# Optimization experiments

Hardware: AMD Instinct MI355X
Metric: run time of the kernel (lower is better)

Reference implementation:

```python
import jax, jax.numpy as jnp
import numpy as np

N = 768      # n_proto (number of class prototypes)
D = 128      # trans_feat_num
H = D // 16  # edge-MLP hidden = 8
A = 312      # semantic attribute dim
INIT_TEMP = 0.1
VTEMP = 10.0
STEMP = 10.0
EPS = 1e-8


def _layer_norm(x, g, b, eps=1e-5):
    m = x.mean(-1, keepdims=True)
    v = ((x - m) ** 2).mean(-1, keepdims=True)
    return (x - m) / jnp.sqrt(v + eps) * g + b


def _instance_norm_rows(x, eps=1e-5):
    # torch InstanceNorm1d on 2D input: unbatched (C, L) -> normalize each row, no affine
    m = x.mean(-1, keepdims=True)
    v = ((x - m) ** 2).mean(-1, keepdims=True)
    return (x - m) / jnp.sqrt(v + eps)


def _init_edge(x, temp):
    # pairwise cosine similarity + row softmax
    nrm = jnp.linalg.norm(x, axis=1)
    sim = (x @ x.T) / jnp.maximum(nrm[:, None] * nrm[None, :], EPS)
    return jax.nn.softmax(sim / temp, axis=-1)


def _edge_update(proto, last_edge, W1, b1, W2, b2, temp):
    n, d = proto.shape
    # O(n^2) pairwise squared differences  -> [n*n, d]
    feat = ((proto[:, None, :] - proto[None, :, :]) ** 2).reshape(n * n, d)
    h = jax.nn.relu(_instance_norm_rows(feat @ W1.T + b1))  # [n*n, H]
    e = jnp.tanh(h @ W2.T + b2).reshape(n, n)
    return jax.nn.softmax(e * (last_edge + EPS) / temp, axis=-1)


def _node_update(proto, last_edge, edge, W, b, g, beta):
    extra = last_edge @ proto          # cross-modal message (dist_injection)
    p = edge @ proto                   # same-modal aggregation
    return jax.nn.relu(_layer_norm((p + extra) @ W.T + b, g, beta)) + p


def setup_inputs() -> dict:
    key = jax.random.key(0)
    ks = jax.random.split(key, 9)
    rn = lambda k, shape, s=1.0: jax.random.normal(k, shape, dtype=jnp.float32) * s
    return {
        "visual_proto": rn(ks[0], (N, D)),
        "semantic_proto": rn(ks[1], (N, D)),
        "attribute": rn(ks[2], (N, A)),
        "Wvn": rn(ks[3], (D, D), 0.08), "bvn": jnp.zeros((D,), jnp.float32),
        "gvn": jnp.ones((D,), jnp.float32), "betavn": jnp.zeros((D,), jnp.float32),
        "Wve1": rn(ks[4], (H, D), 0.1), "bve1": jnp.zeros((H,), jnp.float32),
        "Wve2": rn(ks[5], (1, H), 0.3), "bve2": jnp.zeros((1,), jnp.float32),
        "Wsn": rn(ks[6], (D, D), 0.08), "bsn": jnp.zeros((D,), jnp.float32),
        "gsn": jnp.ones((D,), jnp.float32), "betasn": jnp.zeros((D,), jnp.float32),
        "Wse1": rn(ks[7], (H, D), 0.1), "bse1": jnp.zeros((H,), jnp.float32),
        "Wse2": rn(ks[8], (1, H), 0.3), "bse2": jnp.zeros((1,), jnp.float32),
    }


def reference(visual_proto, semantic_proto, attribute,
              Wvn, bvn, gvn, betavn, Wve1, bve1, Wve2, bve2,
              Wsn, bsn, gsn, betasn, Wse1, bse1, Wse2, bse2):
    ve = _init_edge(visual_proto, INIT_TEMP)
    se = _init_edge(attribute, INIT_TEMP)
    vp = _node_update(visual_proto, se, ve, Wvn, bvn, gvn, betavn)
    ve2 = _edge_update(vp, ve, Wve1, bve1, Wve2, bve2, VTEMP)
    sp = _node_update(semantic_proto, ve2, se, Wsn, bsn, gsn, betasn)
    se2 = _edge_update(sp, se, Wse1, bse1, Wse2, bse2, STEMP)
    return vp, sp, ve2, se2
```

## Files before the change

### kernel.cpp

```cpp
#include <hip/hip_runtime.h>
#include <math.h>

#define NN 768
#define DD 128
#define AA 312
#define HH 8
#define CEPS 1e-8f
#define SMEM_F 5920

typedef __attribute__((ext_vector_type(8))) short s8b;
typedef __attribute__((ext_vector_type(4))) float f4v;

__device__ __forceinline__ float wave_sum(float v) {
    #pragma unroll
    for (int o = 32; o; o >>= 1) v += __shfl_down(v, o, 64);
    return v;
}
__device__ __forceinline__ float wave_max(float v) {
    #pragma unroll
    for (int o = 32; o; o >>= 1) v = fmaxf(v, __shfl_down(v, o, 64));
    return v;
}
__device__ __forceinline__ unsigned short f2bf(float f) {
    unsigned u = __float_as_uint(f);
    u += 0x7FFFu + ((u >> 16) & 1u);
    return (unsigned short)(u >> 16);
}

struct KParams {
    const float *visual, *semantic, *attribute;
    const float *Wvn, *bvn, *gvn, *betavn, *Wve1, *bve1, *Wve2, *bve2;
    const float *Wsn, *bsn, *gsn, *betasn, *Wse1, *bse1, *Wse2, *bse2;
    float *vp, *sp, *ve2, *se2;
    float *simv, *sima, *WvnT, *WsnT, *cvec1, *cvec2;
    float *nrmv, *nrma;
    short *vpb, *spb;
};

__global__ __launch_bounds__(256) void gram_mfma_kernel(KParams p) {
    __shared__ __align__(16) unsigned short AH[64 * 40];
    __shared__ __align__(16) unsigned short AL[64 * 40];
    __shared__ __align__(16) unsigned short BH[64 * 40];
    __shared__ __align__(16) unsigned short BL[64 * 40];
    const int task = blockIdx.x;
    const int tid = threadIdx.x;
    if (task < 288) {
        const bool isv = (task < 144);
        const int tt = isv ? task : task - 144;
        const int bi = tt / 12, bj = tt % 12;
        const float* M = isv ? p.visual : p.attribute;
        float* G = isv ? p.simv : p.sima;
        float* nrm = isv ? p.nrmv : p.nrma;
        const int K = isv ? DD : AA;
        const int i0 = bi * 64, j0 = bj * 64;
        const int w = tid >> 6, lane = tid & 63;
        const int m = lane & 15, q = lane >> 4;
        f4v acc[4] = {{0.f, 0.f, 0.f, 0.f}, {0.f, 0.f, 0.f, 0.f},
                      {0.f, 0.f, 0.f, 0.f}, {0.f, 0.f, 0.f, 0.f}};
        const int nchunk = (K + 31) >> 5;
        const int srow = tid >> 2, sq = (tid & 3) * 8;
        for (int c = 0; c < nchunk; ++c) {
            const int kc = c * 32;
            __syncthreads();
            #pragma unroll
            for (int h = 0; h < 2; ++h) {
                const int col = sq + h * 4;
                float4 a = {0.f, 0.f, 0.f, 0.f}, b = {0.f, 0.f, 0.f, 0.f};
                if (kc + col + 4 <= K) {
                    a = *(const float4*)(M + (size_t)(i0 + srow) * K + kc + col);
                    b = *(const float4*)(M + (size_t)(j0 + srow) * K + kc + col);
                }
                const float av[4] = {a.x, a.y, a.z, a.w};
                const float bv[4] = {b.x, b.y, b.z, b.w};
                #pragma unroll
                for (int e = 0; e < 4; ++e) {
                    const unsigned short ah = f2bf(av[e]);
                    const float ahf = __uint_as_float((unsigned)ah << 16);
                    const unsigned short al = f2bf(av[e] - ahf);
                    const unsigned short bh = f2bf(bv[e]);
                    const float bhf = __uint_as_float((unsigned)bh << 16);
                    const unsigned short bl = f2bf(bv[e] - bhf);
                    AH[srow * 40 + col + e] = ah;
                    AL[srow * 40 + col + e] = al;
                    BH[srow * 40 + col + e] = bh;
                    BL[srow * 40 + col + e] = bl;
                }
            }
            __syncthreads();
            const s8b ah8 = *(const s8b*)&AH[(w * 16 + m) * 40 + q * 8];
            const s8b al8 = *(const s8b*)&AL[(w * 16 + m) * 40 + q * 8];
            #pragma unroll
            for (int jt = 0; jt < 4; ++jt) {
                const s8b bh8 = *(const s8b*)&BH[(jt * 16 + m) * 40 + q * 8];
                const s8b bl8 = *(const s8b*)&BL[(jt * 16 + m) * 40 + q * 8];
                acc[jt] = __builtin_amdgcn_mfma_f32_16x16x32_bf16(ah8, bh8, acc[jt], 0, 0, 0);
                acc[jt] = __builtin_amdgcn_mfma_f32_16x16x32_bf16(ah8, bl8, acc[jt], 0, 0, 0);
                acc[jt] = __builtin_amdgcn_mfma_f32_16x16x32_bf16(al8, bh8, acc[jt], 0, 0, 0);
            }
        }
        #pragma unroll
        for (int jt = 0; jt < 4; ++jt) {
            #pragma unroll
            for (int r = 0; r < 4; ++r) {
                G[(size_t)(i0 + w * 16 + q * 4 + r) * NN + j0 + jt * 16 + m] = acc[jt][r];
                if (bi == bj && jt == w && m == q * 4 + r)
                    nrm[i0 + w * 16 + m] = sqrtf(fmaxf(acc[jt][r], 0.f));
            }
        }
    } else {
        float* smem = (float*)AH;
        const int u = task - 288;
        const float* S = (u >= 16) ? p.Wsn : p.Wvn;
        float* Dt = (u >= 16) ? p.WsnT : p.WvnT;
        const int tile = u & 15;
        const int c0 = (tile & 3) * 32, r0 = (tile >> 2) * 32;
        const int tx = tid & 31, ty = tid >> 5;
        #pragma unroll
        for (int rr = ty; rr < 32; rr += 8)
            smem[rr * 33 + tx] = S[(size_t)(r0 + rr) * DD + c0 + tx];
        __syncthreads();
        #pragma unroll
        for (int rr = ty; rr < 32; rr += 8)
            Dt[(size_t)(c0 + rr) * DD + r0 + tx] = smem[tx * 33 + rr];
    }
}

__device__ void block_softmax768(float* buf, int tid, float* red) {
    const int w = tid >> 6, lane = tid & 63;
    float v0 = buf[tid];
    float v1 = (tid < NN - 512) ? buf[tid + 512] : -3.4e38f;
    float m = wave_max(fmaxf(v0, v1));
    if (lane == 0) red[w] = m;
    __syncthreads();
    m = red[0];
    #pragma unroll
    for (int i = 1; i < 8; ++i) m = fmaxf(m, red[i]);
    float e0 = __expf(v0 - m);
    float e1 = (tid < NN - 512) ? __expf(v1 - m) : 0.f;
    float sw = wave_sum(e0 + e1);
    if (lane == 0) red[8 + w] = sw;
    __syncthreads();
    float s = 0.f;
    #pragma unroll
    for (int i = 0; i < 8; ++i) s += red[8 + i];
    const float inv = 1.f / s;
    buf[tid] = e0 * inv;
    if (tid < NN - 512) buf[tid + 512] = e1 * inv;
    __syncthreads();
}

__device__ void norm_rows(float (*buf)[NN], const float* __restrict__ nrm, int i0, int tid) {
    const float n0 = nrm[i0], n1 = nrm[i0 + 1];
    for (int k = tid; k < NN; k += 512) {
        const float nj = nrm[k];
        buf[0][k] = buf[0][k] * 10.f / fmaxf(n0 * nj, CEPS);
        buf[1][k] = buf[1][k] * 10.f / fmaxf(n1 * nj, CEPS);
    }
}

template <bool SMEP, bool SMEX>
__global__ __launch_bounds__(512) void node_kernel(
    const float* __restrict__ P, const float* __restrict__ EpSrc, const float* __restrict__ ExSrc,
    const float* __restrict__ nrmP, const float* __restrict__ nrmX,
    const float* __restrict__ WT, const float* __restrict__ b, const float* __restrict__ g,
    const float* __restrict__ beta, float* __restrict__ out, const float* __restrict__ W1e,
    short* __restrict__ outb, float* __restrict__ cvec) {
    __shared__ __align__(16) float ep[2][NN], ex[2][NN];
    __shared__ __align__(16) float pp[4][2][DD], xx[4][2][DD];
    __shared__ __align__(16) float qs[2][DD], tps[2][2][DD];
    __shared__ float red[16];
    const int i0 = blockIdx.x * 2;
    const int tid = threadIdx.x;
    const int s = (tid >> 7) & 3, d = tid & 127;
    if (tid < 384) {
        ((float4*)ep)[tid] = ((const float4*)(EpSrc + (size_t)i0 * NN))[tid];
        ((float4*)ex)[tid] = ((const float4*)(ExSrc + (size_t)i0 * NN))[tid];
    }
    __syncthreads();
    if (SMEP) {
        norm_rows(ep, nrmP, i0, tid);
        block_softmax768(ep[0], tid, red);
        block_softmax768(ep[1], tid, red);
    }
    if (SMEX) {
        norm_rows(ex, nrmX, i0, tid);
        block_softmax768(ex[0], tid, red);
        block_softmax768(ex[1], tid, red);
    }
    float p0 = 0.f, x0 = 0.f, p1 = 0.f, x1 = 0.f;
    const int kb = s * 192;
    #pragma unroll 4
    for (int kk = 0; kk < 192; ++kk) {
        const int k = kb + kk;
        const float pv = P[(size_t)k * DD + d];
        p0 = fmaf(ep[0][k], pv, p0);
        x0 = fmaf(ex[0][k], pv, x0);
        p1 = fmaf(ep[1][k], pv, p1);
        x1 = fmaf(ex[1][k], pv, x1);
    }
    pp[s][0][d] = p0; xx[s][0][d] = x0;
    pp[s][1][d] = p1; xx[s][1][d] = x1;
    __syncthreads();
    const int rr = (tid >> 7) & 1;
    float preg = 0.f;
    if (tid < 256) {
        float p = pp[0][rr][d] + pp[1][rr][d] + pp[2][rr][d] + pp[3][rr][d];
        float x = xx[0][rr][d] + xx[1][rr][d] + xx[2][rr][d] + xx[3][rr][d];
        qs[rr][d] = p + x;
        preg = p;
    }
    __syncthreads();
    {
        const int sc = tid >> 8, rr2 = (tid >> 7) & 1;
        float t = (sc == 0) ? b[d] : 0.f;
        const int c0 = sc * 64;
        #pragma unroll 4
        for (int c = c0; c < c0 + 64; ++c) t = fmaf(qs[rr2][c], WT[(size_t)c * DD + d], t);
        tps[sc][rr2][d] = t;
    }
    __syncthreads();
    float tval = 0.f;
    if (tid < 256) tval = tps[0][rr][d] + tps[1][rr][d];
    float sm = wave_sum(tid < 256 ? tval : 0.f);
    if ((tid & 63) == 0) red[tid >> 6] = sm;
    __syncthreads();
    if (tid < 256) tval -= (red[2 * rr] + red[2 * rr + 1]) * (1.f / DD);
    float s2 = wave_sum(tid < 256 ? tval * tval : 0.f);
    if ((tid & 63) == 0) red[8 + (tid >> 6)] = s2;
    __syncthreads();
    if (tid < 256) {
        const float var = (red[8 + 2 * rr] + red[8 + 2 * rr + 1]) * (1.f / DD);
        const float ln = tval * rsqrtf(var + 1e-5f) * g[d] + beta[d];
        const float val = fmaxf(ln, 0.f) + preg;
        out[(size_t)(i0 + rr) * DD + d] = val;
        outb[(size_t)(i0 + rr) * DD + d] = (short)f2bf(val);
        qs[rr][d] = val;
    }
    __syncthreads();
    if (tid < 256) {
        const int row = tid >> 7, r = (tid >> 4) & 7, l16 = tid & 15;
        float ssum = 0.f;
        #pragma unroll
        for (int t = 0; t < 8; ++t) {
            const int k = l16 + 16 * t;
            const float pv = qs[row][k];
            ssum = fmaf(W1e[r * DD + k], pv * pv, ssum);
        }
        #pragma unroll
        for (int o = 8; o; o >>= 1) ssum += __shfl_down(ssum, o, 16);
        if (l16 == 0) cvec[(size_t)(i0 + row) * HH + r] = ssum;
    }
}

__global__ __launch_bounds__(512) void edge_kernel(
    const float* __restrict__ PR, const short* __restrict__ PRb, const float* __restrict__ cvec,
    const float* __restrict__ ELraw, const float* __restrict__ nrmE,
    const float* __restrict__ W1, const float* __restrict__ b1, const float* __restrict__ W2,
    const float* __restrict__ b2, float invtemp, float* __restrict__ out) {
    __shared__ __align__(16) float pi[2][DD];
    __shared__ __align__(16) float w1s[HH * DD];
    __shared__ __align__(16) short a_sw[4 * 64 * 8];
    __shared__ __align__(16) float Ls[2][NN];
    __shared__ __align__(16) float Els[2][NN];
    __shared__ float red[16];
    const int i0 = blockIdx.x * 2;
    const int tid = threadIdx.x;
    const int lane = tid & 63, wave = tid >> 6;
    if (tid < 256) {
        pi[tid >> 7][tid & 127] = PR[(size_t)(i0 + (tid >> 7)) * DD + (tid & 127)];
        ((float4*)w1s)[tid] = ((const float4*)W1)[tid];
    }
    if (tid < 384)
        ((float4*)Els)[tid] = ((const float4*)(ELraw + (size_t)i0 * NN))[tid];
    __syncthreads();
    norm_rows(Els, nrmE, i0, tid);
    block_softmax768(Els[0], tid, red);
    block_softmax768(Els[1], tid, red);
    if (tid < 256) {
        const int t = tid >> 6, m = lane & 15, q2 = lane >> 4;
        const int il = m >> 3, r = m & 7;
        const int kb = t * 32 + q2 * 8;
        s8b av;
        #pragma unroll
        for (int e = 0; e < 8; ++e)
            av[e] = (short)f2bf(pi[il][kb + e] * w1s[r * DD + kb + e]);
        *(s8b*)&a_sw[(t * 64 + lane) * 8] = av;
    }
    __syncthreads();
    s8b af[4];
    #pragma unroll
    for (int t = 0; t < 4; ++t) af[t] = *(const s8b*)&a_sw[(t * 64 + lane) * 8];
    const int q = lane >> 4, n = lane & 15;
    const int rbase = (q & 1) * 4;
    const int il = q >> 1;
    const float4 ci4 = *(const float4*)&cvec[(size_t)(i0 + il) * HH + rbase];
    const float4 b14 = *(const float4*)&b1[rbase];
    const float4 w24 = *(const float4*)&W2[rbase];
    const float b2s = b2[0];
    #pragma unroll
    for (int s = 0; s < 6; ++s) {
        const int j = wave * 96 + s * 16 + n;
        f4v acc = {0.f, 0.f, 0.f, 0.f};
        #pragma unroll
        for (int t = 0; t < 4; ++t) {
            const s8b bf = *(const s8b*)(PRb + (size_t)j * DD + t * 32 + q * 8);
            acc = __builtin_amdgcn_mfma_f32_16x16x32_bf16(af[t], bf, acc, 0, 0, 0);
        }
        const float4 cj = *(const float4*)&cvec[(size_t)j * HH + rbase];
        float z[4];
        z[0] = ci4.x + cj.x - 2.f * acc[0] + b14.x;
        z[1] = ci4.y + cj.y - 2.f * acc[1] + b14.y;
        z[2] = ci4.z + cj.z - 2.f * acc[2] + b14.z;
        z[3] = ci4.w + cj.w - 2.f * acc[3] + b14.w;
        float s1 = z[0] + z[1] + z[2] + z[3];
        float s2 = z[0] * z[0] + z[1] * z[1] + z[2] * z[2] + z[3] * z[3];
        s1 += __shfl_xor(s1, 16, 64);
        s2 += __shfl_xor(s2, 16, 64);
        const float mean = s1 * (1.f / HH);
        const float var = fmaxf(s2 * (1.f / HH) - mean * mean, 0.f);
        const float istd = rsqrtf(var + 1e-5f);
        float a2 = 0.f;
        a2 = fmaf(fmaxf((z[0] - mean) * istd, 0.f), w24.x, a2);
        a2 = fmaf(fmaxf((z[1] - mean) * istd, 0.f), w24.y, a2);
        a2 = fmaf(fmaxf((z[2] - mean) * istd, 0.f), w24.z, a2);
        a2 = fmaf(fmaxf((z[3] - mean) * istd, 0.f), w24.w, a2);
        a2 += __shfl_xor(a2, 16, 64);
        const float tv = tanhf(a2 + b2s);
        const float lv = Els[il][j];
        if ((q & 1) == 0) Ls[il][j] = tv * (lv + CEPS) * invtemp;
    }
    __syncthreads();
    block_softmax768(Ls[0], tid, red);
    block_softmax768(Ls[1], tid, red);
    float* d0 = out + (size_t)i0 * NN;
    float* d1 = out + (size_t)(i0 + 1) * NN;
    d0[tid] = Ls[0][tid];
    d1[tid] = Ls[1][tid];
    if (tid < NN - 512) {
        d0[tid + 512] = Ls[0][tid + 512];
        d1[tid + 512] = Ls[1][tid + 512];
    }
}

extern "C" void kernel_launch(void* const* d_in, const int* in_sizes, int n_in, void* d_out,
                              int out_size, void* d_ws, size_t ws_size, hipStream_t stream) {
    KParams kp;
    kp.visual    = (const float*)d_in[0];
    kp.semantic  = (const float*)d_in[1];
    kp.attribute = (const float*)d_in[2];
    kp.Wvn  = (const float*)d_in[3];
    kp.bvn  = (const float*)d_in[4];
    kp.gvn  = (const float*)d_in[5];
    kp.betavn = (const float*)d_in[6];
    kp.Wve1 = (const float*)d_in[7];
    kp.bve1 = (const float*)d_in[8];
    kp.Wve2 = (const float*)d_in[9];
    kp.bve2 = (const float*)d_in[10];
    kp.Wsn  = (const float*)d_in[11];
    kp.bsn  = (const float*)d_in[12];
    kp.gsn  = (const float*)d_in[13];
    kp.betasn = (const float*)d_in[14];
    kp.Wse1 = (const float*)d_in[15];
    kp.bse1 = (const float*)d_in[16];
    kp.Wse2 = (const float*)d_in[17];
    kp.bse2 = (const float*)d_in[18];

    float* out = (float*)d_out;
    kp.vp  = out;
    kp.sp  = out + 98304;
    kp.ve2 = out + 196608;
    kp.se2 = out + 786432;

    float* ws = (float*)d_ws;
    kp.simv  = ws;
    kp.sima  = ws + 589824;
    kp.WvnT  = ws + 2949120;
    kp.WsnT  = ws + 2965504;
    kp.cvec1 = ws + 2981888;
    kp.cvec2 = ws + 2988032;
    kp.vpb   = (short*)(ws + 2994176);
    kp.spb   = (short*)(ws + 3043328);
    kp.nrmv  = ws + 3092480;
    kp.nrma  = ws + 3093248;

    gram_mfma_kernel<<<320, 256, 0, stream>>>(kp);
    node_kernel<true, true><<<NN / 2, 512, 0, stream>>>(
        kp.visual, kp.simv, kp.sima, kp.nrmv, kp.nrma, kp.WvnT, kp.bvn, kp.gvn, kp.betavn,
        kp.vp, kp.Wve1, kp.vpb, kp.cvec1);
    edge_kernel<<<NN / 2, 512, 0, stream>>>(kp.vp, kp.vpb, kp.cvec1, kp.simv, kp.nrmv, kp.Wve1,
                                            kp.bve1, kp.Wve2, kp.bve2, 0.1f, kp.ve2);
    node_kernel<true, false><<<NN / 2, 512, 0, stream>>>(
        kp.semantic, kp.sima, kp.ve2, kp.nrma, nullptr, kp.WsnT, kp.bsn, kp.gsn, kp.betasn,
        kp.sp, kp.Wse1, kp.spb, kp.cvec2);
    edge_kernel<<<NN / 2, 512, 0, stream>>>(kp.sp, kp.spb, kp.cvec2, kp.sima, kp.nrma, kp.Wse1,
                                            kp.bse1, kp.Wse2, kp.bse2, 0.1f, kp.se2);
}
```

Measured before the change: 190.4 us.

## Fuse edge update with next node update and cache initial edge softmaxes

Merges the first edge-update kernel with the semantic node-update kernel, so the freshly computed ve2 rows feed the node aggregation directly from shared memory instead of a global round trip and a separate launch. The node1 kernel now stores the softmaxed initial edge rows (ve, se) to workspace, so later kernels reload them rather than recomputing the norm and softmax. This cuts one kernel launch and redundant softmax work. In exchange it uses extra global traffic for the cached edges and more LDS per block in the fused kernel, which may reduce occupancy.

```diff
diff --git a/kernel.cpp b/kernel.cpp
--- a/kernel.cpp
+++ b/kernel.cpp
@@ -6,7 +6,6 @@
 #define AA 312
 #define HH 8
 #define CEPS 1e-8f
-#define SMEM_F 5920
 
 typedef __attribute__((ext_vector_type(8))) short s8b;
 typedef __attribute__((ext_vector_type(4))) float f4v;
@@ -33,7 +32,7 @@
     const float *Wsn, *bsn, *gsn, *betasn, *Wse1, *bse1, *Wse2, *bse2;
     float *vp, *sp, *ve2, *se2;
     float *simv, *sima, *WvnT, *WsnT, *cvec1, *cvec2;
-    float *nrmv, *nrma;
+    float *nrmv, *nrma, *ve, *se;
     short *vpb, *spb;
 };
 
@@ -158,35 +157,14 @@
     }
 }
 
-template <bool SMEP, bool SMEX>
-__global__ __launch_bounds__(512) void node_kernel(
-    const float* __restrict__ P, const float* __restrict__ EpSrc, const float* __restrict__ ExSrc,
-    const float* __restrict__ nrmP, const float* __restrict__ nrmX,
-    const float* __restrict__ WT, const float* __restrict__ b, const float* __restrict__ g,
-    const float* __restrict__ beta, float* __restrict__ out, const float* __restrict__ W1e,
-    short* __restrict__ outb, float* __restrict__ cvec) {
-    __shared__ __align__(16) float ep[2][NN], ex[2][NN];
-    __shared__ __align__(16) float pp[4][2][DD], xx[4][2][DD];
-    __shared__ __align__(16) float qs[2][DD], tps[2][2][DD];
-    __shared__ float red[16];
-    const int i0 = blockIdx.x * 2;
-    const int tid = threadIdx.x;
+__device__ void node_core(const float* __restrict__ P, float (*ep)[NN], float (*ex)[NN],
+                          const float* __restrict__ WT, const float* __restrict__ b,
+                          const float* __restrict__ g, const float* __restrict__ beta,
+                          float* __restrict__ out, const float* __restrict__ W1e,
+                          short* __restrict__ outb, float* __restrict__ cvec, int i0, int tid,
+                          float (*pp)[2][DD], float (*xx)[2][DD], float (*qs)[DD],
+                          float (*tps)[2][DD], float* red) {
     const int s = (tid >> 7) & 3, d = tid & 127;
-    if (tid < 384) {
-        ((float4*)ep)[tid] = ((const float4*)(EpSrc + (size_t)i0 * NN))[tid];
-        ((float4*)ex)[tid] = ((const float4*)(ExSrc + (size_t)i0 * NN))[tid];
-    }
-    __syncthreads();
-    if (SMEP) {
-        norm_rows(ep, nrmP, i0, tid);
-        block_softmax768(ep[0], tid, red);
-        block_softmax768(ep[1], tid, red);
-    }
-    if (SMEX) {
-        norm_rows(ex, nrmX, i0, tid);
-        block_softmax768(ex[0], tid, red);
-        block_softmax768(ex[1], tid, red);
-    }
     float p0 = 0.f, x0 = 0.f, p1 = 0.f, x1 = 0.f;
     const int kb = s * 192;
     #pragma unroll 4
@@ -252,30 +230,39 @@
     }
 }
 
-__global__ __launch_bounds__(512) void edge_kernel(
-    const float* __restrict__ PR, const short* __restrict__ PRb, const float* __restrict__ cvec,
-    const float* __restrict__ ELraw, const float* __restrict__ nrmE,
-    const float* __restrict__ W1, const float* __restrict__ b1, const float* __restrict__ W2,
-    const float* __restrict__ b2, float invtemp, float* __restrict__ out) {
-    __shared__ __align__(16) float pi[2][DD];
-    __shared__ __align__(16) float w1s[HH * DD];
-    __shared__ __align__(16) short a_sw[4 * 64 * 8];
-    __shared__ __align__(16) float Ls[2][NN];
-    __shared__ __align__(16) float Els[2][NN];
+__global__ __launch_bounds__(512) void node1_kernel(KParams p) {
+    __shared__ __align__(16) float ep[2][NN], ex[2][NN];
+    __shared__ __align__(16) float pp[4][2][DD], xx[4][2][DD];
+    __shared__ __align__(16) float qs[2][DD], tps[2][2][DD];
     __shared__ float red[16];
     const int i0 = blockIdx.x * 2;
     const int tid = threadIdx.x;
+    if (tid < 384) {
+        ((float4*)ep)[tid] = ((const float4*)(p.simv + (size_t)i0 * NN))[tid];
+        ((float4*)ex)[tid] = ((const float4*)(p.sima + (size_t)i0 * NN))[tid];
+    }
+    __syncthreads();
+    norm_rows(ep, p.nrmv, i0, tid);
+    norm_rows(ex, p.nrma, i0, tid);
+    block_softmax768(ep[0], tid, red);
+    block_softmax768(ep[1], tid, red);
+    block_softmax768(ex[0], tid, red);
+    block_softmax768(ex[1], tid, red);
+    if (tid < 384) {
+        ((float4*)(p.ve + (size_t)i0 * NN))[tid] = ((float4*)ep)[tid];
+        ((float4*)(p.se + (size_t)i0 * NN))[tid] = ((float4*)ex)[tid];
+    }
+    node_core(p.visual, ep, ex, p.WvnT, p.bvn, p.gvn, p.betavn, p.vp, p.Wve1, p.vpb, p.cvec1,
+              i0, tid, pp, xx, qs, tps, red);
+}
+
+__device__ void edge_core(const float* __restrict__ PR, const short* __restrict__ PRb,
+                          const float* __restrict__ cvec, const float* __restrict__ W1,
+                          const float* __restrict__ b1, const float* __restrict__ W2,
+                          const float* __restrict__ b2, float invtemp, int i0, int tid,
+                          float (*pi)[DD], float* w1s, short* a_sw, float (*Lv)[NN],
+                          float (*Ls)[NN], float* red) {
     const int lane = tid & 63, wave = tid >> 6;
-    if (tid < 256) {
-        pi[tid >> 7][tid & 127] = PR[(size_t)(i0 + (tid >> 7)) * DD + (tid & 127)];
-        ((float4*)w1s)[tid] = ((const float4*)W1)[tid];
-    }
-    if (tid < 384)
-        ((float4*)Els)[tid] = ((const float4*)(ELraw + (size_t)i0 * NN))[tid];
-    __syncthreads();
-    norm_rows(Els, nrmE, i0, tid);
-    block_softmax768(Els[0], tid, red);
-    block_softmax768(Els[1], tid, red);
     if (tid < 256) {
         const int t = tid >> 6, m = lane & 15, q2 = lane >> 4;
         const int il = m >> 3, r = m & 7;
@@ -326,14 +313,63 @@
         a2 = fmaf(fmaxf((z[3] - mean) * istd, 0.f), w24.w, a2);
         a2 += __shfl_xor(a2, 16, 64);
         const float tv = tanhf(a2 + b2s);
-        const float lv = Els[il][j];
+        const float lv = Lv[il][j];
         if ((q & 1) == 0) Ls[il][j] = tv * (lv + CEPS) * invtemp;
     }
     __syncthreads();
     block_softmax768(Ls[0], tid, red);
     block_softmax768(Ls[1], tid, red);
-    float* d0 = out + (size_t)i0 * NN;
-    float* d1 = out + (size_t)(i0 + 1) * NN;
+}
+
+__global__ __launch_bounds__(512) void edge_node_kernel(KParams p) {
+    __shared__ __align__(16) float pi[2][DD];
+    __shared__ __align__(16) float w1s[HH * DD];
+    __shared__ __align__(16) short a_sw[4 * 64 * 8];
+    __shared__ __align__(16) float Lv[2][NN];
+    __shared__ __align__(16) float Ls[2][NN];
+    __shared__ __align__(16) float ep[2][NN];
+    __shared__ __align__(16) float pp[4][2][DD], xx[4][2][DD];
+    __shared__ __align__(16) float qs[2][DD], tps[2][2][DD];
+    __shared__ float red[16];
+    const int i0 = blockIdx.x * 2;
+    const int tid = threadIdx.x;
+    if (tid < 256) {
+        pi[tid >> 7][tid & 127] = p.vp[(size_t)(i0 + (tid >> 7)) * DD + (tid & 127)];
+        ((float4*)w1s)[tid] = ((const float4*)p.Wve1)[tid];
+    }
+    if (tid < 384) {
+        ((float4*)Lv)[tid] = ((const float4*)(p.ve + (size_t)i0 * NN))[tid];
+        ((float4*)ep)[tid] = ((const float4*)(p.se + (size_t)i0 * NN))[tid];
+    }
+    __syncthreads();
+    edge_core(p.vp, p.vpb, p.cvec1, p.Wve1, p.bve1, p.Wve2, p.bve2, 0.1f, i0, tid, pi, w1s,
+              a_sw, Lv, Ls, red);
+    if (tid < 384)
+        ((float4*)(p.ve2 + (size_t)i0 * NN))[tid] = ((float4*)Ls)[tid];
+    node_core(p.semantic, ep, Ls, p.WsnT, p.bsn, p.gsn, p.betasn, p.sp, p.Wse1, p.spb,
+              p.cvec2, i0, tid, pp, xx, qs, tps, red);
+}
+
+__global__ __launch_bounds__(512) void edge2_kernel(KParams p) {
+    __shared__ __align__(16) float pi[2][DD];
+    __shared__ __align__(16) float w1s[HH * DD];
+    __shared__ __align__(16) short a_sw[4 * 64 * 8];
+    __shared__ __align__(16) float Lv[2][NN];
+    __shared__ __align__(16) float Ls[2][NN];
+    __shared__ float red[16];
+    const int i0 = blockIdx.x * 2;
+    const int tid = threadIdx.x;
+    if (tid < 256) {
+        pi[tid >> 7][tid & 127] = p.sp[(size_t)(i0 + (tid >> 7)) * DD + (tid & 127)];
+        ((float4*)w1s)[tid] = ((const float4*)p.Wse1)[tid];
+    }
+    if (tid < 384)
+        ((float4*)Lv)[tid] = ((const float4*)(p.se + (size_t)i0 * NN))[tid];
+    __syncthreads();
+    edge_core(p.sp, p.spb, p.cvec2, p.Wse1, p.bse1, p.Wse2, p.bse2, 0.1f, i0, tid, pi, w1s,
+              a_sw, Lv, Ls, red);
+    float* d0 = p.se2 + (size_t)i0 * NN;
+    float* d1 = p.se2 + (size_t)(i0 + 1) * NN;
     d0[tid] = Ls[0][tid];
     d1[tid] = Ls[1][tid];
     if (tid < NN - 512) {
@@ -374,6 +410,8 @@
     float* ws = (float*)d_ws;
     kp.simv  = ws;
     kp.sima  = ws + 589824;
+    kp.ve    = ws + 1179648;
+    kp.se    = ws + 1769472;
     kp.WvnT  = ws + 2949120;
     kp.WsnT  = ws + 2965504;
     kp.cvec1 = ws + 2981888;
@@ -384,14 +422,7 @@
     kp.nrma  = ws + 3093248;
 
     gram_mfma_kernel<<<320, 256, 0, stream>>>(kp);
-    node_kernel<true, true><<<NN / 2, 512, 0, stream>>>(
-        kp.visual, kp.simv, kp.sima, kp.nrmv, kp.nrma, kp.WvnT, kp.bvn, kp.gvn, kp.betavn,
-        kp.vp, kp.Wve1, kp.vpb, kp.cvec1);
-    edge_kernel<<<NN / 2, 512, 0, stream>>>(kp.vp, kp.vpb, kp.cvec1, kp.simv, kp.nrmv, kp.Wve1,
-                                            kp.bve1, kp.Wve2, kp.bve2, 0.1f, kp.ve2);
-    node_kernel<true, false><<<NN / 2, 512, 0, stream>>>(
-        kp.semantic, kp.sima, kp.ve2, kp.nrma, nullptr, kp.WsnT, kp.bsn, kp.gsn, kp.betasn,
-        kp.sp, kp.Wse1, kp.spb, kp.cvec2);
-    edge_kernel<<<NN / 2, 512, 0, stream>>>(kp.sp, kp.spb, kp.cvec2, kp.sima, kp.nrma, kp.Wse1,
-                                            kp.bse1, kp.Wse2, kp.bse2, 0.1f, kp.se2);
-}
+    node1_kernel<<<NN / 2, 512, 0, stream>>>(kp);
+    edge_node_kernel<<<NN / 2, 512, 0, stream>>>(kp);
+    edge2_kernel<<<NN / 2, 512, 0, stream>>>(kp);
+}
```

Result: faster. 184.0 us (-3.4%).
